# Optimization experiments

Measured on AMD Instinct MI355X. Metric: run time of the kernel, lower is better.

## Reference

```python
import jax, jax.numpy as jnp
import numpy as np

B, N, C, H = 4, 1024, 1024, 16
HD = C // H  # 64
THETA = 10000.0


def _rope_cos_sin(n, hd, theta):
    # classic 1D RoPE cache; [n, hd] with each freq repeated twice (interleaved pairs)
    inv_freq = 1.0 / theta ** (jnp.arange(0, hd, 2, dtype=jnp.float32) / hd)
    t = jnp.arange(n, dtype=jnp.float32)
    freqs = t[:, None] * inv_freq[None, :]              # [n, hd/2]
    cos = jnp.repeat(jnp.cos(freqs), 2, axis=-1)        # [n, hd]
    sin = jnp.repeat(jnp.sin(freqs), 2, axis=-1)
    # original clones & forces row 0 to identity rotation (already true since t=0)
    cos = cos.at[0].set(1.0)
    sin = sin.at[0].set(0.0)
    return cos, sin


def _rotate_half(x):
    # interleaved rotate-half: (x0,x1,x2,x3,...) -> (-x1,x0,-x3,x2,...)
    x1 = x[..., 0::2]
    x2 = x[..., 1::2]
    return jnp.stack((-x2, x1), axis=-1).reshape(x.shape)


def setup_inputs() -> dict:
    key = jax.random.key(0)
    ks = jax.random.split(key, 5)
    s = 0.02
    return {
        "x": jax.random.normal(ks[0], (B, N, C), dtype=jnp.float32),
        "qkv_w": jax.random.normal(ks[1], (3 * C, C), dtype=jnp.float32) * s,
        "qkv_b": jax.random.normal(ks[2], (3 * C,), dtype=jnp.float32) * s,
        "proj_w": jax.random.normal(ks[3], (C, C), dtype=jnp.float32) * s,
        "proj_b": jax.random.normal(ks[4], (C,), dtype=jnp.float32) * s,
    }


def reference(x, qkv_w, qkv_b, proj_w, proj_b):
    b, n, c = x.shape
    h, hd = H, HD
    qkv = x @ qkv_w.T + qkv_b                              # [b, n, 3c]
    qkv = qkv.reshape(b, n, 3, h, hd).transpose(2, 0, 3, 1, 4)  # [3, b, h, n, hd]
    q, k, v = qkv[0], qkv[1], qkv[2]
    scale = hd ** -0.5
    q = q * scale                                          # explicit pre-scale (as in source)
    cos, sin = _rope_cos_sin(n, hd, THETA)                 # [n, hd]
    cos = cos[None, None]                                  # broadcast over b, h
    sin = sin[None, None]
    q = q * cos + _rotate_half(q) * sin
    k = k * cos + _rotate_half(k) * sin
    # F.scaled_dot_product_attention also applies its default 1/sqrt(hd) scale
    logits = jnp.einsum('bhqd,bhkd->bhqk', q, k) * scale   # [b, h, n, n]
    attn = jax.nn.softmax(logits, axis=-1)
    out = jnp.einsum('bhqk,bhkd->bhqd', attn, v)           # [b, h, n, hd]
    out = out.transpose(0, 2, 1, 3).reshape(b, n, c)
    return out @ proj_w.T + proj_b
```

## Files before the change

kernel.cpp:

```cpp
#include <hip/hip_runtime.h>
#include <hip/hip_bf16.h>
#include <stdint.h>

#define DEVI __device__ __forceinline__

typedef __attribute__((ext_vector_type(8))) short short8;
typedef __attribute__((ext_vector_type(4))) short short4v;
typedef __attribute__((ext_vector_type(4))) float floatx4;

DEVI ushort f2bf(float f) {
  union { float f; uint32_t u; } v; v.f = f;
  uint32_t u = v.u;
  uint32_t r = (u + 0x7FFFu + ((u >> 16) & 1u)) >> 16;
  return (ushort)r;
}
DEVI ushort f2bf_fast(float f) {
  union { float f; uint32_t u; } v; v.f = f;
  return (ushort)((v.u + 0x8000u) >> 16);
}
DEVI float bf2f(ushort h) {
  union { uint32_t u; float f; } v; v.u = ((uint32_t)h) << 16;
  return v.f;
}
DEVI void gld_lds16(const void* g, void* l) {
  __builtin_amdgcn_global_load_lds(
      (const __attribute__((address_space(1))) unsigned int*)g,
      (__attribute__((address_space(3))) unsigned int*)l, 16, 0, 0);
}

__global__ __launch_bounds__(256, 4) void cast_all(
    const float* __restrict__ x, const float* __restrict__ w1,
    const float* __restrict__ w2, ushort* __restrict__ xb,
    ushort* __restrict__ w1b, ushort* __restrict__ w2b) {
  const int N1 = 4096 * 1024, N2 = 3072 * 1024, N3 = 1024 * 1024;
  int i = (blockIdx.x * 256 + threadIdx.x) * 4;
  const int total = N1 + N2 + N3;
  int stride = gridDim.x * 256 * 4;
  for (; i < total; i += stride) {
    const float* src; ushort* dst; int off;
    if (i < N1) { src = x; dst = xb; off = i; }
    else if (i < N1 + N2) { src = w1; dst = w1b; off = i - N1; }
    else { src = w2; dst = w2b; off = i - N1 - N2; }
    float4 v = *(const float4*)(src + off);
    ushort4 o;
    o.x = f2bf(v.x); o.y = f2bf(v.y); o.z = f2bf(v.z); o.w = f2bf(v.w);
    *(ushort4*)(dst + off) = o;
  }
}

__global__ __launch_bounds__(256, 4) void rope_table(float2* __restrict__ tab) {
  int id = blockIdx.x * 256 + threadIdx.x;
  int j = id & 31, n = id >> 5;
  float inv = powf(10000.0f, -(float)(2 * j) / 64.0f);
  float fr = (float)n * inv;
  tab[id] = make_float2(cosf(fr), sinf(fr));
}

__global__ __launch_bounds__(256, 3) void gemm_qkv(
    const ushort* __restrict__ A, const ushort* __restrict__ Bm,
    const float* __restrict__ bias, const float2* __restrict__ tab,
    ushort* __restrict__ Qb, ushort* __restrict__ Kb,
    ushort* __restrict__ Vsrc) {
  const int K = 1024;
  __shared__ char lds[3][16384];
  char* L0 = &lds[0][0];
  const int tid = threadIdx.x;
  const int w = tid >> 6, lane = tid & 63;

  const int bid = blockIdx.x;
  const int xcd = bid & 7, i5 = bid >> 3;
  const int lm = i5 & 7, ln = i5 >> 3;
  const int mt = (xcd & 3) * 8 + lm;
  const int nt = (xcd >> 2) * 12 + ln;
  const int m0 = mt * 128, n0 = nt * 128;

  const int wm = (w >> 1) * 64, wn = (w & 1) * 64;
  const int lrow = lane & 15, lk2 = (lane >> 4) * 16;

  const ushort* agp = A + (size_t)(m0 + w * 32 + (lane >> 2)) * K + (lane & 3) * 8;
  const ushort* bgp = Bm + (size_t)(n0 + w * 32 + (lane >> 2)) * K + (lane & 3) * 8;
  const int stoff = w * 2048 + lane * 16;

  auto STAGE = [&](const int base) {
    char* L = L0 + base;
    gld_lds16(agp, L + stoff);
    gld_lds16(agp + 16 * K, L + stoff + 1024);
    gld_lds16(bgp, L + 8192 + stoff);
    gld_lds16(bgp + 16 * K, L + 8192 + stoff + 1024);
    agp += 32; bgp += 32;
  };

  floatx4 acc[4][4] = {};

  auto TILE = [&](const int base) {
    const char* L = L0 + base;
    short8 af[4], bf[4];
#pragma unroll
    for (int t = 0; t < 4; ++t) {
      af[t] = *(const short8*)(L + (wm + t * 16 + lrow) * 64 + lk2);
      bf[t] = *(const short8*)(L + 8192 + (wn + t * 16 + lrow) * 64 + lk2);
    }
#pragma unroll
    for (int i = 0; i < 4; ++i)
#pragma unroll
      for (int j = 0; j < 4; ++j)
        acc[i][j] = __builtin_amdgcn_mfma_f32_16x16x32_bf16(af[i], bf[j], acc[i][j], 0, 0, 0);
  };

  STAGE(0);
  STAGE(16384);
  int bT = 0, bS = 32768;

  for (int t = 0; t < 31; ++t) {
    asm volatile("s_waitcnt vmcnt(4)" ::: "memory");
    __builtin_amdgcn_s_barrier();
    __builtin_amdgcn_sched_barrier(0);
    if (t < 30) STAGE(bS);
    __builtin_amdgcn_sched_barrier(0);
    TILE(bT);
    __builtin_amdgcn_sched_barrier(0);
    bT += 16384; if (bT == 49152) bT = 0;
    bS += 16384; if (bS == 49152) bS = 0;
  }
  asm volatile("s_waitcnt vmcnt(0)" ::: "memory");
  __builtin_amdgcn_s_barrier();
  __builtin_amdgcn_sched_barrier(0);
  TILE(bT);

  const int role = n0 >> 10;
  const float sc = (1.0f / 64.0f) * 1.44269504088896f;
#pragma unroll
  for (int i = 0; i < 4; ++i) {
    int mrow = m0 + wm + i * 16 + (lane >> 4) * 4;
#pragma unroll
    for (int j = 0; j < 4; ++j) {
      int ncol = n0 + wn + j * 16 + (lane & 15);
      float bv = bias[ncol];
      int cm = ncol & 1023;
      int h = cm >> 6, d = cm & 63;
#pragma unroll
      for (int r = 0; r < 4; ++r) {
        float v = acc[i][j][r] + bv;
        int row = mrow + r;
        int b = row >> 10, n = row & 1023;
        if (role == 2) {
          Vsrc[(size_t)row * 1024 + cm] = f2bf(v);
        } else {
          float p = __shfl_xor(v, 1);
          float2 cs = tab[n * 32 + (d >> 1)];
          float o = (d & 1) ? (v * cs.x + p * cs.y) : (v * cs.x - p * cs.y);
          if (role == 0) o *= sc;
          ushort* dst = (role == 0) ? Qb : Kb;
          dst[((size_t)(b * 16 + h) * 1024 + n) * 64 + d] = f2bf(o);
        }
      }
    }
  }
}

__global__ __launch_bounds__(256, 3) void gemm_proj(
    const ushort* __restrict__ A, const ushort* __restrict__ Bm,
    const float* __restrict__ bias, float* __restrict__ Cout) {
  const int K = 1024;
  __shared__ char lds[3][16384];
  char* L0 = &lds[0][0];
  const int tid = threadIdx.x;
  const int w = tid >> 6, lane = tid & 63;

  const int bid = blockIdx.x;
  const int xcd = bid & 7, i5 = bid >> 3;
  const int lm = i5 & 7, ln = i5 >> 3;
  const int mt = (xcd & 3) * 8 + lm;
  const int nt = (xcd >> 2) * 4 + ln;
  const int m0 = mt * 128, n0 = nt * 128;

  const int wm = (w >> 1) * 64, wn = (w & 1) * 64;
  const int lrow = lane & 15, lk2 = (lane >> 4) * 16;

  const ushort* agp = A + (size_t)(m0 + w * 32 + (lane >> 2)) * K + (lane & 3) * 8;
  const ushort* bgp = Bm + (size_t)(n0 + w * 32 + (lane >> 2)) * K + (lane & 3) * 8;
  const int stoff = w * 2048 + lane * 16;

  auto STAGE = [&](const int base) {
    char* L = L0 + base;
    gld_lds16(agp, L + stoff);
    gld_lds16(agp + 16 * K, L + stoff + 1024);
    gld_lds16(bgp, L + 8192 + stoff);
    gld_lds16(bgp + 16 * K, L + 8192 + stoff + 1024);
    agp += 32; bgp += 32;
  };

  floatx4 acc[4][4] = {};

  auto TILE = [&](const int base) {
    const char* L = L0 + base;
    short8 af[4], bf[4];
#pragma unroll
    for (int t = 0; t < 4; ++t) {
      af[t] = *(const short8*)(L + (wm + t * 16 + lrow) * 64 + lk2);
      bf[t] = *(const short8*)(L + 8192 + (wn + t * 16 + lrow) * 64 + lk2);
    }
#pragma unroll
    for (int i = 0; i < 4; ++i)
#pragma unroll
      for (int j = 0; j < 4; ++j)
        acc[i][j] = __builtin_amdgcn_mfma_f32_16x16x32_bf16(af[i], bf[j], acc[i][j], 0, 0, 0);
  };

  STAGE(0);
  STAGE(16384);
  int bT = 0, bS = 32768;

  for (int t = 0; t < 31; ++t) {
    asm volatile("s_waitcnt vmcnt(4)" ::: "memory");
    __builtin_amdgcn_s_barrier();
    __builtin_amdgcn_sched_barrier(0);
    if (t < 30) STAGE(bS);
    __builtin_amdgcn_sched_barrier(0);
    TILE(bT);
    __builtin_amdgcn_sched_barrier(0);
    bT += 16384; if (bT == 49152) bT = 0;
    bS += 16384; if (bS == 49152) bS = 0;
  }
  asm volatile("s_waitcnt vmcnt(0)" ::: "memory");
  __builtin_amdgcn_s_barrier();
  __builtin_amdgcn_sched_barrier(0);
  TILE(bT);

#pragma unroll
  for (int i = 0; i < 4; ++i) {
    int mrow = m0 + wm + i * 16 + (lane >> 4) * 4;
#pragma unroll
    for (int j = 0; j < 4; ++j) {
      int ncol = n0 + wn + j * 16 + (lane & 15);
      float bv = bias[ncol];
#pragma unroll
      for (int r = 0; r < 4; ++r)
        Cout[(size_t)(mrow + r) * 1024 + ncol] = acc[i][j][r] + bv;
    }
  }
}

__global__ __launch_bounds__(256, 4) void v_trans(
    const ushort* __restrict__ Vsrc, ushort* __restrict__ Vt) {
  __shared__ ushort t[64][72];
  int bh = blockIdx.y, ntile = blockIdx.x;
  int b = bh >> 4, h = bh & 15;
  int n0 = ntile * 64;
  int tid = threadIdx.x;
  int r = tid >> 2, cc = (tid & 3) * 16;
  const ushort* src = Vsrc + (size_t)(b * 1024 + n0 + r) * 1024 + h * 64 + cc;
  *(short8*)(&t[r][cc]) = *(const short8*)(src);
  *(short8*)(&t[r][cc + 8]) = *(const short8*)(src + 8);
  __syncthreads();
  int d = tid >> 2;
  ushort outv[16];
#pragma unroll
  for (int i = 0; i < 16; ++i) outv[i] = t[cc + i][d];
  ushort* dst = Vt + (size_t)bh * 65536 + (size_t)d * 1024 + n0 + cc;
  *(short8*)(dst) = *(const short8*)(outv);
  *(short8*)(dst + 8) = *(const short8*)(outv + 8);
}

__global__ __launch_bounds__(256, 4) void attn(
    const ushort* __restrict__ Q, const ushort* __restrict__ Kc,
    const ushort* __restrict__ Vt, ushort* __restrict__ AO) {
  __shared__ char lds[2][16384];
  char* ldsbase = &lds[0][0];
  int id = blockIdx.x;
  int bh = id & 63, qi = id >> 6;
  int b = bh >> 4, h = bh & 15;
  int q0 = qi * 64;
  int tid = threadIdx.x, w = tid >> 6, lane = tid & 63;
  int l15 = lane & 15, g = lane >> 4;
  const ushort* Qbh = Q + (size_t)bh * 65536;
  const char* Kbh = (const char*)(Kc + (size_t)bh * 65536);
  const char* Vbh = (const char*)(Vt + (size_t)bh * 65536);

  short8 qf[2];
#pragma unroll
  for (int ks = 0; ks < 2; ++ks)
    qf[ks] = *(const short8*)(Qbh + (size_t)(q0 + w * 16 + l15) * 64 + ks * 32 + g * 8);

  int kaddr[8];
#pragma unroll
  for (int ks = 0; ks < 2; ++ks)
#pragma unroll
    for (int nt = 0; nt < 4; ++nt) {
      int row = nt * 16 + l15;
      kaddr[ks * 4 + nt] = (row * 128 + ks * 64 + g * 16) ^ ((row & 7) << 4);
    }
  int vaddr[16];
#pragma unroll
  for (int ch = 0; ch < 2; ++ch)
#pragma unroll
    for (int dt = 0; dt < 4; ++dt)
#pragma unroll
      for (int hf = 0; hf < 2; ++hf) {
        int row = dt * 16 + l15;
        vaddr[(ch * 4 + dt) * 2 + hf] =
            8192 + ((row * 128 + ch * 64 + hf * 32 + g * 8) ^ ((row & 7) << 4));
      }

  const int d0 = w * 2048 + lane * 16;
  const int d1 = d0 + 1024;
  const int r0 = d0 >> 7, r1 = d1 >> 7;
  const int s0 = d0 ^ ((r0 & 7) << 4), s1 = d1 ^ ((r1 & 7) << 4);
  const char* pK0 = Kbh + s0;
  const char* pK1 = Kbh + s1;
  const char* pV0 = Vbh + r0 * 2048 + (s0 & 127);
  const char* pV1 = Vbh + r1 * 2048 + (s1 & 127);

  auto STAGE = [&](const int B) {
    gld_lds16(pK0, ldsbase + B + d0);
    gld_lds16(pK1, ldsbase + B + d1);
    gld_lds16(pV0, ldsbase + B + 8192 + d0);
    gld_lds16(pV1, ldsbase + B + 8192 + d1);
    pK0 += 8192; pK1 += 8192; pV0 += 128; pV1 += 128;
  };

  floatx4 oacc[4] = {};
  float lrun = 0.f;

  auto TILE = [&](const int B) {
    floatx4 sacc[4] = {};
    __builtin_amdgcn_s_setprio(1);
#pragma unroll
    for (int ks = 0; ks < 2; ++ks) {
      short8 kf[4];
#pragma unroll
      for (int nt = 0; nt < 4; ++nt)
        kf[nt] = *(const short8*)(ldsbase + B + kaddr[ks * 4 + nt]);
#pragma unroll
      for (int nt = 0; nt < 4; ++nt)
        sacc[nt] = __builtin_amdgcn_mfma_f32_16x16x32_bf16(kf[nt], qf[ks], sacc[nt], 0, 0, 0);
    }
    __builtin_amdgcn_s_setprio(0);

    float rs = 0.f;
#pragma unroll
    for (int nt = 0; nt < 4; ++nt)
#pragma unroll
      for (int r = 0; r < 4; ++r) {
        float p = __builtin_amdgcn_exp2f(sacc[nt][r]);
        sacc[nt][r] = p;
        rs += p;
      }
    lrun += rs;

    short8 pa[2];
#pragma unroll
    for (int ch = 0; ch < 2; ++ch)
#pragma unroll
      for (int r = 0; r < 4; ++r) {
        pa[ch][r] = (short)f2bf_fast(sacc[2 * ch][r]);
        pa[ch][r + 4] = (short)f2bf_fast(sacc[2 * ch + 1][r]);
      }

    __builtin_amdgcn_s_setprio(1);
#pragma unroll
    for (int ch = 0; ch < 2; ++ch)
#pragma unroll
      for (int dt = 0; dt < 4; ++dt) {
        short4v va = *(const short4v*)(ldsbase + B + vaddr[(ch * 4 + dt) * 2]);
        short4v vb = *(const short4v*)(ldsbase + B + vaddr[(ch * 4 + dt) * 2 + 1]);
        short8 vf = __builtin_shufflevector(va, vb, 0, 1, 2, 3, 4, 5, 6, 7);
        oacc[dt] = __builtin_amdgcn_mfma_f32_16x16x32_bf16(pa[ch], vf, oacc[dt], 0, 0, 0);
      }
    __builtin_amdgcn_s_setprio(0);
  };

  STAGE(0);
  asm volatile("s_waitcnt vmcnt(0)" ::: "memory");
  __builtin_amdgcn_s_barrier();
  __builtin_amdgcn_sched_barrier(0);

  for (int kt = 0; kt < 16; kt += 2) {
    STAGE(16384);
    __builtin_amdgcn_sched_barrier(0);
    TILE(0);
    asm volatile("s_waitcnt vmcnt(0)" ::: "memory");
    __builtin_amdgcn_s_barrier();
    __builtin_amdgcn_sched_barrier(0);

    if (kt + 2 < 16) STAGE(0);
    __builtin_amdgcn_sched_barrier(0);
    TILE(16384);
    asm volatile("s_waitcnt vmcnt(0)" ::: "memory");
    __builtin_amdgcn_s_barrier();
    __builtin_amdgcn_sched_barrier(0);
  }

  lrun += __shfl_xor(lrun, 16);
  lrun += __shfl_xor(lrun, 32);
  float linv = 1.0f / lrun;
  float linvR[4];
#pragma unroll
  for (int r = 0; r < 4; ++r) linvR[r] = __shfl(linv, g * 4 + r);
#pragma unroll
  for (int r = 0; r < 4; ++r) {
    int nseq = q0 + w * 16 + g * 4 + r;
#pragma unroll
    for (int dt = 0; dt < 4; ++dt) {
      int d = dt * 16 + l15;
      AO[(size_t)(b * 1024 + nseq) * 1024 + h * 64 + d] = f2bf(oacc[dt][r] * linvR[r]);
    }
  }
}

extern "C" void kernel_launch(void* const* d_in, const int* in_sizes, int n_in,
                              void* d_out, int out_size, void* d_ws, size_t ws_size,
                              hipStream_t stream) {
  const float* x = (const float*)d_in[0];
  const float* qkv_w = (const float*)d_in[1];
  const float* qkv_b = (const float*)d_in[2];
  const float* proj_w = (const float*)d_in[3];
  const float* proj_b = (const float*)d_in[4];
  float* out = (float*)d_out;

  char* ws = (char*)d_ws;
  size_t off = 0;
  auto alloc = [&](size_t bytes) -> void* {
    void* p = ws + off;
    off += (bytes + 255) & ~(size_t)255;
    return p;
  };
  ushort* xb = (ushort*)alloc(4096ull * 1024 * 2);
  ushort* wqkvb = (ushort*)alloc(3072ull * 1024 * 2);
  ushort* wprojb = (ushort*)alloc(1024ull * 1024 * 2);
  ushort* Qb = (ushort*)alloc(64ull * 1024 * 64 * 2);
  ushort* Kb = (ushort*)alloc(64ull * 1024 * 64 * 2);
  ushort* Vsrc = (ushort*)alloc(4096ull * 1024 * 2);
  ushort* Vt = (ushort*)alloc(64ull * 1024 * 64 * 2);
  ushort* AO = (ushort*)alloc(4096ull * 1024 * 2);
  float2* tab = (float2*)alloc(1024ull * 32 * sizeof(float2));

  cast_all<<<2048, 256, 0, stream>>>(x, qkv_w, proj_w, xb, wqkvb, wprojb);
  rope_table<<<128, 256, 0, stream>>>(tab);

  gemm_qkv<<<768, 256, 0, stream>>>(xb, wqkvb, qkv_b, tab, Qb, Kb, Vsrc);

  dim3 gv(16, 64);
  v_trans<<<gv, 256, 0, stream>>>(Vsrc, Vt);

  attn<<<1024, 256, 0, stream>>>(Qb, Kb, Vt, AO);

  gemm_proj<<<256, 256, 0, stream>>>(AO, wprojb, proj_b, out);
}
```

Before: 103.6 us.

## Rewrite QKV GEMM with 256x256 tiles, 8 waves, swizzled LDS and phased pipeline

The QKV projection GEMM moves from 128x128 tiles with 4 waves and a 3-stage LDS ring to 256x256 tiles with 8 waves, 128KB of LDS, and double-buffered K=64 slices. Global-to-LDS loads are interleaved with MFMA phases, using s_setprio to favour the math waves, and the LDS layout is XOR-swizzled to avoid bank conflicts. The aim is more data reuse per loaded byte and better overlap of memory and compute. The cost is that the grid shrinks to 192 blocks, below the CU count, so occupancy drops and some CUs may sit idle.

```diff
diff --git a/kernel.cpp b/kernel.cpp
--- a/kernel.cpp
+++ b/kernel.cpp
@@ -56,85 +56,105 @@
   tab[id] = make_float2(cosf(fr), sinf(fr));
 }
 
-__global__ __launch_bounds__(256, 3) void gemm_qkv(
+__global__ __launch_bounds__(512, 2) void gemm_qkv(
     const ushort* __restrict__ A, const ushort* __restrict__ Bm,
     const float* __restrict__ bias, const float2* __restrict__ tab,
     ushort* __restrict__ Qb, ushort* __restrict__ Kb,
     ushort* __restrict__ Vsrc) {
-  const int K = 1024;
-  __shared__ char lds[3][16384];
-  char* L0 = &lds[0][0];
+  __shared__ __align__(16) char lds[131072];
   const int tid = threadIdx.x;
-  const int w = tid >> 6, lane = tid & 63;
+  const int wid = tid >> 6, lane = tid & 63;
+  const int wm = wid >> 2, wn = wid & 3;
+  const int lrow = lane & 15, g = lane >> 4;
 
   const int bid = blockIdx.x;
-  const int xcd = bid & 7, i5 = bid >> 3;
-  const int lm = i5 & 7, ln = i5 >> 3;
-  const int mt = (xcd & 3) * 8 + lm;
-  const int nt = (xcd >> 2) * 12 + ln;
-  const int m0 = mt * 128, n0 = nt * 128;
-
-  const int wm = (w >> 1) * 64, wn = (w & 1) * 64;
-  const int lrow = lane & 15, lk2 = (lane >> 4) * 16;
-
-  const ushort* agp = A + (size_t)(m0 + w * 32 + (lane >> 2)) * K + (lane & 3) * 8;
-  const ushort* bgp = Bm + (size_t)(n0 + w * 32 + (lane >> 2)) * K + (lane & 3) * 8;
-  const int stoff = w * 2048 + lane * 16;
-
-  auto STAGE = [&](const int base) {
-    char* L = L0 + base;
-    gld_lds16(agp, L + stoff);
-    gld_lds16(agp + 16 * K, L + stoff + 1024);
-    gld_lds16(bgp, L + 8192 + stoff);
-    gld_lds16(bgp + 16 * K, L + 8192 + stoff + 1024);
-    agp += 32; bgp += 32;
-  };
-
-  floatx4 acc[4][4] = {};
-
-  auto TILE = [&](const int base) {
-    const char* L = L0 + base;
-    short8 af[4], bf[4];
-#pragma unroll
-    for (int t = 0; t < 4; ++t) {
-      af[t] = *(const short8*)(L + (wm + t * 16 + lrow) * 64 + lk2);
-      bf[t] = *(const short8*)(L + 8192 + (wn + t * 16 + lrow) * 64 + lk2);
-    }
-#pragma unroll
-    for (int i = 0; i < 4; ++i)
-#pragma unroll
-      for (int j = 0; j < 4; ++j)
-        acc[i][j] = __builtin_amdgcn_mfma_f32_16x16x32_bf16(af[i], bf[j], acc[i][j], 0, 0, 0);
-  };
-
-  STAGE(0);
-  STAGE(16384);
-  int bT = 0, bS = 32768;
-
-  for (int t = 0; t < 31; ++t) {
-    asm volatile("s_waitcnt vmcnt(4)" ::: "memory");
-    __builtin_amdgcn_s_barrier();
-    __builtin_amdgcn_sched_barrier(0);
-    if (t < 30) STAGE(bS);
-    __builtin_amdgcn_sched_barrier(0);
-    TILE(bT);
-    __builtin_amdgcn_sched_barrier(0);
-    bT += 16384; if (bT == 49152) bT = 0;
-    bS += 16384; if (bS == 49152) bS = 0;
-  }
-  asm volatile("s_waitcnt vmcnt(0)" ::: "memory");
+  const int xcd = bid / 24, loc = bid % 24;
+  const int mt = (xcd & 1) * 8 + (loc & 7);
+  const int nt = (xcd >> 1) * 3 + (loc >> 3);
+  const int m0 = mt * 256, n0 = nt * 256;
+
+  const int sw16 = ((g ^ ((lrow >> 1) & 3)) << 4);
+  const int aBase = (wm * 128 + lrow) * 64 + sw16;
+  const int bBase = 65536 + (wn * 64 + lrow) * 64 + sw16;
+
+  const int i2base = wid * 2;
+  const int swsrc = (((lane & 3) ^ ((lane >> 3) & 3)) << 4);
+  const char* Asrc = (const char*)A + (size_t)(m0 + (lane >> 2)) * 2048 + swsrc;
+  const char* Bsrc = (const char*)Bm + (size_t)(n0 + (lane >> 2)) * 2048 + swsrc;
+  const int ldst = lane * 16;
+
+  auto SU = [&](int op, int T, int kh) {
+    const char* s = (op ? Bsrc : Asrc) + (size_t)i2base * 16 * 2048 + T * 128 + kh * 64;
+    char* d = lds + op * 65536 + (T & 1) * 32768 + kh * 16384 + i2base * 1024 + ldst;
+    gld_lds16(s, d);
+    gld_lds16(s + 16 * 2048, d + 1024);
+  };
+
+  floatx4 acc[8][4] = {};
+  short8 bf0, bf1, bf2, bf3;
+
+#define MM(i_, j_, af_, bf_) \
+  acc[(i_)][(j_)] = __builtin_amdgcn_mfma_f32_16x16x32_bf16(af_, bf_, acc[(i_)][(j_)], 0, 0, 0)
+
+#define PHASE(D, KS, MH, ...) do { \
+  const char* Lp_ = lds + (D) * 32768 + (KS) * 16384; \
+  short8 af0_ = *(const short8*)(Lp_ + aBase + ((MH) * 64 + 0) * 64); \
+  short8 af1_ = *(const short8*)(Lp_ + aBase + ((MH) * 64 + 16) * 64); \
+  short8 af2_ = *(const short8*)(Lp_ + aBase + ((MH) * 64 + 32) * 64); \
+  short8 af3_ = *(const short8*)(Lp_ + aBase + ((MH) * 64 + 48) * 64); \
+  if ((MH) == 0) { \
+    bf0 = *(const short8*)(Lp_ + bBase + 0 * 64); \
+    bf1 = *(const short8*)(Lp_ + bBase + 16 * 64); \
+    bf2 = *(const short8*)(Lp_ + bBase + 32 * 64); \
+    bf3 = *(const short8*)(Lp_ + bBase + 48 * 64); \
+  } \
+  __VA_ARGS__; \
+  __builtin_amdgcn_sched_barrier(0); \
+  __builtin_amdgcn_s_barrier(); \
+  __builtin_amdgcn_sched_barrier(0); \
+  __builtin_amdgcn_s_setprio(1); \
+  MM((MH)*4+0, 0, af0_, bf0); MM((MH)*4+0, 1, af0_, bf1); \
+  MM((MH)*4+0, 2, af0_, bf2); MM((MH)*4+0, 3, af0_, bf3); \
+  MM((MH)*4+1, 0, af1_, bf0); MM((MH)*4+1, 1, af1_, bf1); \
+  MM((MH)*4+1, 2, af1_, bf2); MM((MH)*4+1, 3, af1_, bf3); \
+  MM((MH)*4+2, 0, af2_, bf0); MM((MH)*4+2, 1, af2_, bf1); \
+  MM((MH)*4+2, 2, af2_, bf2); MM((MH)*4+2, 3, af2_, bf3); \
+  MM((MH)*4+3, 0, af3_, bf0); MM((MH)*4+3, 1, af3_, bf1); \
+  MM((MH)*4+3, 2, af3_, bf2); MM((MH)*4+3, 3, af3_, bf3); \
+  __builtin_amdgcn_s_setprio(0); \
+  __builtin_amdgcn_sched_barrier(0); \
+  asm volatile("s_waitcnt vmcnt(6)" ::: "memory"); \
+  __builtin_amdgcn_s_barrier(); \
+  __builtin_amdgcn_sched_barrier(0); \
+} while (0)
+
+  SU(0, 0, 0); SU(1, 0, 0); SU(0, 0, 1); SU(1, 0, 1); SU(0, 1, 0); SU(1, 1, 0);
+  asm volatile("s_waitcnt vmcnt(8)" ::: "memory");
   __builtin_amdgcn_s_barrier();
   __builtin_amdgcn_sched_barrier(0);
-  TILE(bT);
+
+  for (int it = 0; it < 8; ++it) {
+    const int t = 2 * it;
+    PHASE(0, 0, 0, SU(0, t + 1, 1));
+    PHASE(0, 0, 1, SU(1, t + 1, 1));
+    PHASE(0, 1, 0, if (t + 2 < 16) SU(0, t + 2, 0));
+    PHASE(0, 1, 1, if (t + 2 < 16) SU(1, t + 2, 0));
+    PHASE(1, 0, 0, if (t + 2 < 16) SU(0, t + 2, 1));
+    PHASE(1, 0, 1, if (t + 2 < 16) SU(1, t + 2, 1));
+    PHASE(1, 1, 0, if (t + 3 < 16) SU(0, t + 3, 0));
+    PHASE(1, 1, 1, if (t + 3 < 16) SU(1, t + 3, 0));
+  }
+#undef PHASE
+#undef MM
 
   const int role = n0 >> 10;
   const float sc = (1.0f / 64.0f) * 1.44269504088896f;
 #pragma unroll
-  for (int i = 0; i < 4; ++i) {
-    int mrow = m0 + wm + i * 16 + (lane >> 4) * 4;
+  for (int i = 0; i < 8; ++i) {
+    int mrow = m0 + wm * 128 + i * 16 + g * 4;
 #pragma unroll
     for (int j = 0; j < 4; ++j) {
-      int ncol = n0 + wn + j * 16 + (lane & 15);
+      int ncol = n0 + wn * 64 + j * 16 + lrow;
       float bv = bias[ncol];
       int cm = ncol & 1023;
       int h = cm >> 6, d = cm & 63;
@@ -438,7 +458,7 @@
   cast_all<<<2048, 256, 0, stream>>>(x, qkv_w, proj_w, xb, wqkvb, wprojb);
   rope_table<<<128, 256, 0, stream>>>(tab);
 
-  gemm_qkv<<<768, 256, 0, stream>>>(xb, wqkvb, qkv_b, tab, Qb, Kb, Vsrc);
+  gemm_qkv<<<192, 512, 0, stream>>>(xb, wqkvb, qkv_b, tab, Qb, Kb, Vsrc);
 
   dim3 gv(16, 64);
   v_trans<<<gv, 256, 0, stream>>>(Vsrc, Vt);
```

Measured after the change: 116.8 us. +12.8%, slower.

## Swizzle LDS tiles and switch QKV GEMM to double-buffered pipeline

Applied to the files above, without the earlier changes.

The QKV projection GEMM drops its three-stage LDS ring for two separate A/B double buffers. It applies an XOR swizzle to the 16-byte chunks on both the global-to-LDS store and the fragment reads, to remove LDS bank conflicts. It also raises the occupancy hint from 3 to 4 blocks, since each block now uses less LDS. The trade-off is that each step now waits for all outstanding loads (vmcnt(0)) before its barrier, so loads get less time to overlap with compute than in the deeper pipeline.

```diff
diff --git a/kernel.cpp b/kernel.cpp
--- a/kernel.cpp
+++ b/kernel.cpp
@@ -56,14 +56,13 @@
   tab[id] = make_float2(cosf(fr), sinf(fr));
 }
 
-__global__ __launch_bounds__(256, 3) void gemm_qkv(
+__global__ __launch_bounds__(256, 4) void gemm_qkv(
     const ushort* __restrict__ A, const ushort* __restrict__ Bm,
     const float* __restrict__ bias, const float2* __restrict__ tab,
     ushort* __restrict__ Qb, ushort* __restrict__ Kb,
     ushort* __restrict__ Vsrc) {
-  const int K = 1024;
-  __shared__ char lds[3][16384];
-  char* L0 = &lds[0][0];
+  __shared__ __align__(16) char As[2][8192];
+  __shared__ __align__(16) char Bs[2][8192];
   const int tid = threadIdx.x;
   const int w = tid >> 6, lane = tid & 63;
 
@@ -75,30 +74,30 @@
   const int m0 = mt * 128, n0 = nt * 128;
 
   const int wm = (w >> 1) * 64, wn = (w & 1) * 64;
-  const int lrow = lane & 15, lk2 = (lane >> 4) * 16;
-
-  const ushort* agp = A + (size_t)(m0 + w * 32 + (lane >> 2)) * K + (lane & 3) * 8;
-  const ushort* bgp = Bm + (size_t)(n0 + w * 32 + (lane >> 2)) * K + (lane & 3) * 8;
-  const int stoff = w * 2048 + lane * 16;
-
-  auto STAGE = [&](const int base) {
-    char* L = L0 + base;
-    gld_lds16(agp, L + stoff);
-    gld_lds16(agp + 16 * K, L + stoff + 1024);
-    gld_lds16(bgp, L + 8192 + stoff);
-    gld_lds16(bgp + 16 * K, L + 8192 + stoff + 1024);
-    agp += 32; bgp += 32;
+  const int lrow = lane & 15, g = lane >> 4;
+  const int swrd = (g ^ ((lrow >> 1) & 3)) << 4;
+
+  const int swsrc = (((lane & 3) ^ ((lane >> 3) & 3)) << 4);
+  const char* aG = (const char*)A + (size_t)(m0 + w * 32 + (lane >> 2)) * 2048 + swsrc;
+  const char* bG = (const char*)Bm + (size_t)(n0 + w * 32 + (lane >> 2)) * 2048 + swsrc;
+  const int ldst = w * 2048 + lane * 16;
+
+  auto STAGE = [&](const int buf) {
+    gld_lds16(aG, &As[buf][0] + ldst);
+    gld_lds16(aG + 16 * 2048, &As[buf][0] + ldst + 1024);
+    gld_lds16(bG, &Bs[buf][0] + ldst);
+    gld_lds16(bG + 16 * 2048, &Bs[buf][0] + ldst + 1024);
+    aG += 64; bG += 64;
   };
 
   floatx4 acc[4][4] = {};
 
-  auto TILE = [&](const int base) {
-    const char* L = L0 + base;
+  auto TILE = [&](const int buf) {
     short8 af[4], bf[4];
 #pragma unroll
     for (int t = 0; t < 4; ++t) {
-      af[t] = *(const short8*)(L + (wm + t * 16 + lrow) * 64 + lk2);
-      bf[t] = *(const short8*)(L + 8192 + (wn + t * 16 + lrow) * 64 + lk2);
+      af[t] = *(const short8*)(&As[buf][0] + (wm + t * 16 + lrow) * 64 + swrd);
+      bf[t] = *(const short8*)(&Bs[buf][0] + (wn + t * 16 + lrow) * 64 + swrd);
     }
 #pragma unroll
     for (int i = 0; i < 4; ++i)
@@ -108,24 +107,25 @@
   };
 
   STAGE(0);
-  STAGE(16384);
-  int bT = 0, bS = 32768;
-
-  for (int t = 0; t < 31; ++t) {
-    asm volatile("s_waitcnt vmcnt(4)" ::: "memory");
-    __builtin_amdgcn_s_barrier();
-    __builtin_amdgcn_sched_barrier(0);
-    if (t < 30) STAGE(bS);
-    __builtin_amdgcn_sched_barrier(0);
-    TILE(bT);
-    __builtin_amdgcn_sched_barrier(0);
-    bT += 16384; if (bT == 49152) bT = 0;
-    bS += 16384; if (bS == 49152) bS = 0;
-  }
   asm volatile("s_waitcnt vmcnt(0)" ::: "memory");
   __builtin_amdgcn_s_barrier();
   __builtin_amdgcn_sched_barrier(0);
-  TILE(bT);
+
+  for (int t = 0; t < 32; t += 2) {
+    STAGE(1);
+    __builtin_amdgcn_sched_barrier(0);
+    TILE(0);
+    asm volatile("s_waitcnt vmcnt(0)" ::: "memory");
+    __builtin_amdgcn_s_barrier();
+    __builtin_amdgcn_sched_barrier(0);
+
+    if (t + 2 < 32) STAGE(0);
+    __builtin_amdgcn_sched_barrier(0);
+    TILE(1);
+    asm volatile("s_waitcnt vmcnt(0)" ::: "memory");
+    __builtin_amdgcn_s_barrier();
+    __builtin_amdgcn_sched_barrier(0);
+  }
 
   const int role = n0 >> 10;
   const float sc = (1.0f / 64.0f) * 1.44269504088896f;
```

New measurement: 104.7 us. Within noise of the previous version (+1.0%).
